# Kernel tuning notes

Hardware: AMD Instinct MI355X
Metric: run time of the kernel (lower is better)

Reference implementation:

```python
import jax, jax.numpy as jnp
import numpy as np

NUM_HIDDEN = 128
NUM_IN = 256
NUM_HEADS = 4
B, T, N, K = 4, 32, 96, 30


def setup_inputs() -> dict:
    key = jax.random.key(0)
    ks = jax.random.split(key, 7)
    return {
        "h_V": jax.random.normal(ks[0], (B, T, N, NUM_HIDDEN), dtype=jnp.float32),
        "h_EV": jax.random.normal(ks[1], (B, T, N, K, NUM_IN), dtype=jnp.float32),
        "mask_attend": jax.random.randint(ks[2], (B, T, N, K), 0, 2, dtype=jnp.int32),
        "Wq": jax.random.normal(ks[3], (NUM_HIDDEN, NUM_HIDDEN), dtype=jnp.float32) / np.sqrt(NUM_HIDDEN),
        "Wk": jax.random.normal(ks[4], (NUM_IN, NUM_HIDDEN), dtype=jnp.float32) / np.sqrt(NUM_IN),
        "Wv": jax.random.normal(ks[5], (NUM_IN, NUM_HIDDEN), dtype=jnp.float32) / np.sqrt(NUM_IN),
        "Wo": jax.random.normal(ks[6], (NUM_HIDDEN, NUM_HIDDEN), dtype=jnp.float32) / np.sqrt(NUM_HIDDEN),
    }


def reference(h_V, h_EV, mask_attend, Wq, Wk, Wv, Wo):
    b, t, n, k = h_EV.shape[:4]
    h = NUM_HEADS
    d = NUM_HIDDEN // h
    # projections
    Q = (h_V @ Wq).reshape(b, t, n, h, d)            # [B,T,N,H,d]
    Kp = (h_EV @ Wk).reshape(b, t, n, k, h, d)       # [B,T,N,K,H,d]
    V = (h_EV @ Wv).reshape(b, t, n, k, h, d)        # [B,T,N,K,H,d]
    # per-node neighbor attention logits [B,T,N,H,K]
    logits = jnp.einsum('btnhd,btnkhd->btnhk', Q, Kp) / jnp.sqrt(jnp.float32(d))
    neg_inf = jnp.finfo(jnp.float32).min
    mask = mask_attend[:, :, :, None, :]             # [B,T,N,1,K] -> broadcast over heads
    logits = jnp.where(mask > 0, logits, neg_inf)
    attend = jax.nn.softmax(logits, axis=-1)
    attend = attend * mask.astype(jnp.float32)
    # combine values: [B,T,N,H,d]
    out = jnp.einsum('btnhk,btnkhd->btnhd', attend, V).reshape(b, t, n, NUM_HIDDEN)
    return out @ Wo
```

## Files before the change

kernel.cpp:

```cpp
#include <hip/hip_runtime.h>
#include <hip/hip_bf16.h>
#include <cfloat>
#include <math.h>

constexpr int SITES = 12288;
constexpr int KNB   = 30;
constexpr int CIN   = 256;
#define RSQRT_D 0.17677669529663689f

typedef short bf16x8 __attribute__((ext_vector_type(8)));
typedef float f32x4  __attribute__((ext_vector_type(4)));

__device__ inline unsigned short f2bs(float x) {
    __hip_bfloat16 b = __float2bfloat16(x);
    return *(unsigned short*)&b;
}
__device__ inline float bs2f(unsigned short u) {
    unsigned int v = (unsigned int)u << 16;
    float f;
    __builtin_memcpy(&f, &v, 4);
    return f;
}
__device__ inline unsigned int pack2(float a, float b) {
    return (unsigned int)f2bs(a) | ((unsigned int)f2bs(b) << 16);
}

__global__ __launch_bounds__(256) void precompute_w(
    const float* __restrict__ Wq, const float* __restrict__ Wk,
    const float* __restrict__ Wv, const float* __restrict__ Wo,
    unsigned short* __restrict__ Mt, unsigned short* __restrict__ W3t) {
    int gid = blockIdx.x * 256 + threadIdx.x;
    if (gid < 131072) {
        int p = gid >> 7;
        int i = gid & 127;
        int h = p >> 8;
        int c = p & 255;
        const float4* wq = (const float4*)(Wq + (size_t)i * 128 + h * 32);
        const float4* wk = (const float4*)(Wk + (size_t)c * 128 + h * 32);
        float s = 0.f;
        #pragma unroll
        for (int d = 0; d < 8; ++d) {
            float4 a = wq[d], b = wk[d];
            s += a.x * b.x; s += a.y * b.y; s += a.z * b.z; s += a.w * b.w;
        }
        Mt[gid] = f2bs(s);
    } else {
        int o = gid - 131072;
        int p = o >> 7;
        int j = o & 127;
        int h = p >> 8;
        int c = p & 255;
        const float* wv = Wv + (size_t)c * 128 + h * 32;
        const float* wo = Wo + (size_t)(h * 32) * 128 + j;
        float s = 0.f;
        #pragma unroll
        for (int d = 0; d < 32; ++d)
            s += wv[d] * wo[(size_t)d * 128];
        W3t[(size_t)j * 1024 + p] = f2bs(s);
    }
}

template <bool OUT_BF16, bool A_F32>
__global__ __launch_bounds__(256) void gemm_bt_bf16(
    const void* __restrict__ Aptr, const unsigned short* __restrict__ Bt,
    void* __restrict__ C, int M, int N, int K) {
    constexpr int BM = 64, BN = 128, BK = 32, PAD = 8;
    constexpr int NT = BN / 16;
    __shared__ unsigned short As[BM][BK + PAD];
    __shared__ unsigned short Bs[BN][BK + PAD];
    const int tid  = threadIdx.x;
    const int wave = tid >> 6;
    const int lane = tid & 63;
    const int quad = lane >> 4;
    const int l16  = lane & 15;
    const int bm0 = blockIdx.x * BM;
    const int bn0 = blockIdx.y * BN;

    f32x4 acc[NT];
    #pragma unroll
    for (int j = 0; j < NT; ++j) acc[j] = (f32x4){0.f, 0.f, 0.f, 0.f};

    for (int kk = 0; kk < K; kk += BK) {
        {
            int row = tid >> 2, off = (tid & 3) * 8;
            if (A_F32) {
                const float* Af = (const float*)Aptr;
                const float4* src = (const float4*)&Af[(size_t)(bm0 + row) * K + kk + off];
                float4 a0 = src[0], a1 = src[1];
                uint4 p;
                p.x = pack2(a0.x, a0.y); p.y = pack2(a0.z, a0.w);
                p.z = pack2(a1.x, a1.y); p.w = pack2(a1.z, a1.w);
                *(uint4*)&As[row][off] = p;
            } else {
                const unsigned short* Ab = (const unsigned short*)Aptr;
                *(uint4*)&As[row][off] =
                    *(const uint4*)&Ab[(size_t)(bm0 + row) * K + kk + off];
            }
        }
        #pragma unroll
        for (int i = 0; i < 2; ++i) {
            int c2 = tid * 2 + i;
            int brow = c2 >> 2, boff = (c2 & 3) * 8;
            *(uint4*)&Bs[brow][boff] =
                *(const uint4*)&Bt[(size_t)(bn0 + brow) * K + kk + boff];
        }
        __syncthreads();
        bf16x8 af = *(const bf16x8*)&As[wave * 16 + l16][quad * 8];
        #pragma unroll
        for (int j = 0; j < NT; ++j) {
            bf16x8 bf = *(const bf16x8*)&Bs[j * 16 + l16][quad * 8];
            acc[j] = __builtin_amdgcn_mfma_f32_16x16x32_bf16(af, bf, acc[j], 0, 0, 0);
        }
        __syncthreads();
    }
    int row0 = bm0 + wave * 16 + quad * 4;
    #pragma unroll
    for (int j = 0; j < NT; ++j) {
        int col = bn0 + j * 16 + l16;
        #pragma unroll
        for (int r = 0; r < 4; ++r) {
            if (OUT_BF16)
                ((unsigned short*)C)[(size_t)(row0 + r) * N + col] = f2bs(acc[j][r]);
            else
                ((float*)C)[(size_t)(row0 + r) * N + col] = acc[j][r];
        }
    }
}

__global__ __launch_bounds__(256) void attn_kernel(
    const float* __restrict__ hEV, const int* __restrict__ mask,
    const unsigned short* __restrict__ qt, unsigned short* __restrict__ evb) {
    __shared__ unsigned short evS[KNB * CIN];
    __shared__ float qS[1024];
    __shared__ float logitsL[4 * 32];
    __shared__ float attendL[4 * 32];
    __shared__ int   activeS[32];
    __shared__ int   naS;

    const int s = blockIdx.x;
    const int tid = threadIdx.x;
    const int lane = tid & 63;
    const int wv = tid >> 6;
    const int hw = lane >> 5;
    const int sl = lane & 31;

    if (tid < 64) {
        int mk = (tid < KNB) ? mask[(size_t)s * KNB + tid] : 0;
        unsigned long long bal = __ballot(mk > 0);
        if (tid == 0) naS = __popcll(bal);
        if (mk > 0) activeS[__popcll(bal & ((1ull << tid) - 1))] = tid;
    } else if (tid < 192) {
        int t2 = tid - 64;
        uint4 u = ((const uint4*)(qt + (size_t)s * 1024))[t2];
        float f[8];
        f[0] = bs2f(u.x & 0xffff); f[1] = bs2f(u.x >> 16);
        f[2] = bs2f(u.y & 0xffff); f[3] = bs2f(u.y >> 16);
        f[4] = bs2f(u.z & 0xffff); f[5] = bs2f(u.z >> 16);
        f[6] = bs2f(u.w & 0xffff); f[7] = bs2f(u.w >> 16);
        *(float4*)&qS[t2 * 8]     = *(float4*)&f[0];
        *(float4*)&qS[t2 * 8 + 4] = *(float4*)&f[4];
    }
    __syncthreads();

    float qf[4][8];
    #pragma unroll
    for (int h = 0; h < 4; ++h) {
        *(float4*)&qf[h][0] = *(const float4*)&qS[h * 256 + sl * 8];
        *(float4*)&qf[h][4] = *(const float4*)&qS[h * 256 + sl * 8 + 4];
    }
    const int na = naS;

    for (int r = wv * 2 + hw; r < na; r += 8) {
        int k = activeS[r];
        const float* row = hEV + (size_t)s * (KNB * CIN) + (size_t)k * CIN + sl * 8;
        float4 v0 = *(const float4*)row;
        float4 v1 = *(const float4*)(row + 4);

        uint4 p;
        p.x = pack2(v0.x, v0.y); p.y = pack2(v0.z, v0.w);
        p.z = pack2(v1.x, v1.y); p.w = pack2(v1.z, v1.w);
        *(uint4*)&evS[r * CIN + sl * 8] = p;

        float l[4];
        #pragma unroll
        for (int h = 0; h < 4; ++h) {
            l[h] = v0.x * qf[h][0] + v0.y * qf[h][1] + v0.z * qf[h][2] + v0.w * qf[h][3]
                 + v1.x * qf[h][4] + v1.y * qf[h][5] + v1.z * qf[h][6] + v1.w * qf[h][7];
        }
        #pragma unroll
        for (int m = 1; m < 32; m <<= 1) {
            #pragma unroll
            for (int h = 0; h < 4; ++h) l[h] += __shfl_xor(l[h], m, 64);
        }
        if (sl == 0) {
            #pragma unroll
            for (int h = 0; h < 4; ++h) logitsL[h * 32 + r] = l[h] * RSQRT_D;
        }
    }
    __syncthreads();

    {
        float lg = (lane < na) ? logitsL[wv * 32 + lane] : -FLT_MAX;
        float mx = lg;
        #pragma unroll
        for (int m = 1; m < 64; m <<= 1) mx = fmaxf(mx, __shfl_xor(mx, m, 64));
        float e = (lane < na) ? __expf(lg - mx) : 0.f;
        float sm = e;
        #pragma unroll
        for (int m = 1; m < 64; m <<= 1) sm += __shfl_xor(sm, m, 64);
        if (lane < na) attendL[wv * 32 + lane] = e / sm;
    }
    __syncthreads();

    float a0 = 0.f, a1 = 0.f, a2 = 0.f, a3 = 0.f;
    for (int r = 0; r < na; ++r) {
        float evv = bs2f(evS[r * CIN + tid]);
        a0 = fmaf(attendL[r], evv, a0);
        a1 = fmaf(attendL[32 + r], evv, a1);
        a2 = fmaf(attendL[64 + r], evv, a2);
        a3 = fmaf(attendL[96 + r], evv, a3);
    }
    size_t ob = (size_t)s * 1024 + tid;
    evb[ob]       = f2bs(a0);
    evb[ob + 256] = f2bs(a1);
    evb[ob + 512] = f2bs(a2);
    evb[ob + 768] = f2bs(a3);
}

extern "C" void kernel_launch(void* const* d_in, const int* in_sizes, int n_in,
                              void* d_out, int out_size, void* d_ws, size_t ws_size,
                              hipStream_t stream) {
    const float* hV   = (const float*)d_in[0];
    const float* hEV  = (const float*)d_in[1];
    const int*   mask = (const int*)d_in[2];
    const float* Wq   = (const float*)d_in[3];
    const float* Wk   = (const float*)d_in[4];
    const float* Wv   = (const float*)d_in[5];
    const float* Wo   = (const float*)d_in[6];
    float* out = (float*)d_out;

    unsigned short* ws = (unsigned short*)d_ws;
    unsigned short* Mt   = ws;
    unsigned short* W3t  = ws + 131072;
    unsigned short* qt   = ws + 262144;
    unsigned short* evb  = qt + (size_t)SITES * 1024;
    size_t need = ((size_t)262144 + 2 * (size_t)SITES * 1024) * 2;
    if (ws_size < need) return;

    precompute_w<<<dim3(1024), dim3(256), 0, stream>>>(Wq, Wk, Wv, Wo, Mt, W3t);

    gemm_bt_bf16<true, true><<<dim3(SITES / 64, 1024 / 128), dim3(256), 0, stream>>>(
        hV, Mt, qt, SITES, 1024, 128);

    attn_kernel<<<dim3(SITES), dim3(256), 0, stream>>>(hEV, mask, qt, evb);

    gemm_bt_bf16<false, false><<<dim3(SITES / 64, 1), dim3(256), 0, stream>>>(
        evb, W3t, out, SITES, 128, 1024);
}
```

Baseline: 511.9 us.

## Fuse attention with output projection using one wave per site and online softmax

Replaces the per-site attention kernel and the separate output GEMM with a single kernel. Each wave handles four sites in turn, streaming the active neighbor rows with a one-ahead prefetch and an online softmax that only rescales when the running max moves by more than a threshold. The per-site bf16 attention result stays in swizzled shared memory and feeds MFMA against W3t in the same block, so the evb intermediate no longer goes through global memory. In exchange the softmax becomes approximate-online, each wave works through its sites serially, and W3t is reloaded from global memory by every block.

```diff
diff --git a/kernel.cpp b/kernel.cpp
--- a/kernel.cpp
+++ b/kernel.cpp
@@ -127,104 +127,116 @@
     }
 }
 
-__global__ __launch_bounds__(256) void attn_kernel(
+__global__ __launch_bounds__(256) void attn_out_fused(
     const float* __restrict__ hEV, const int* __restrict__ mask,
-    const unsigned short* __restrict__ qt, unsigned short* __restrict__ evb) {
-    __shared__ unsigned short evS[KNB * CIN];
-    __shared__ float qS[1024];
-    __shared__ float logitsL[4 * 32];
-    __shared__ float attendL[4 * 32];
-    __shared__ int   activeS[32];
-    __shared__ int   naS;
-
-    const int s = blockIdx.x;
-    const int tid = threadIdx.x;
+    const unsigned short* __restrict__ qt, const unsigned short* __restrict__ W3t,
+    float* __restrict__ out) {
+    __shared__ __align__(16) unsigned short evbS[16 * 1024];
+    const int tid  = threadIdx.x;
     const int lane = tid & 63;
-    const int wv = tid >> 6;
-    const int hw = lane >> 5;
-    const int sl = lane & 31;
-
-    if (tid < 64) {
-        int mk = (tid < KNB) ? mask[(size_t)s * KNB + tid] : 0;
+    const int wv   = tid >> 6;
+    const int s0   = blockIdx.x * 16;
+
+    for (int si = 0; si < 4; ++si) {
+        const int site = wv * 4 + si;
+        const int s = s0 + site;
+
+        int mk = (lane < KNB) ? mask[(size_t)s * KNB + lane] : 0;
         unsigned long long bal = __ballot(mk > 0);
-        if (tid == 0) naS = __popcll(bal);
-        if (mk > 0) activeS[__popcll(bal & ((1ull << tid) - 1))] = tid;
-    } else if (tid < 192) {
-        int t2 = tid - 64;
-        uint4 u = ((const uint4*)(qt + (size_t)s * 1024))[t2];
-        float f[8];
-        f[0] = bs2f(u.x & 0xffff); f[1] = bs2f(u.x >> 16);
-        f[2] = bs2f(u.y & 0xffff); f[3] = bs2f(u.y >> 16);
-        f[4] = bs2f(u.z & 0xffff); f[5] = bs2f(u.z >> 16);
-        f[6] = bs2f(u.w & 0xffff); f[7] = bs2f(u.w >> 16);
-        *(float4*)&qS[t2 * 8]     = *(float4*)&f[0];
-        *(float4*)&qS[t2 * 8 + 4] = *(float4*)&f[4];
+        unsigned mw = (unsigned)bal & 0x3FFFFFFFu;
+        int na = __popc(mw);
+
+        float qf[4][4];
+        const unsigned short* qrow = qt + (size_t)s * 1024;
+        #pragma unroll
+        for (int h = 0; h < 4; ++h) {
+            ushort4 u = *(const ushort4*)&qrow[h * 256 + lane * 4];
+            qf[h][0] = bs2f(u.x); qf[h][1] = bs2f(u.y);
+            qf[h][2] = bs2f(u.z); qf[h][3] = bs2f(u.w);
+        }
+
+        float mh[4], lh[4], acc[4][4];
+        #pragma unroll
+        for (int h = 0; h < 4; ++h) {
+            mh[h] = -3.0e38f; lh[h] = 0.f;
+            acc[h][0] = acc[h][1] = acc[h][2] = acc[h][3] = 0.f;
+        }
+
+        const float* base = hEV + (size_t)s * (KNB * CIN) + lane * 4;
+        unsigned lmw = mw;
+        float4 cur = {0,0,0,0}, nxt = {0,0,0,0};
+        if (na > 0) {
+            int k = __builtin_ctz(lmw); lmw &= lmw - 1;
+            cur = *(const float4*)(base + (size_t)k * CIN);
+        }
+        for (int r = 0; r < na; ++r) {
+            if (r + 1 < na) {
+                int kn = __builtin_ctz(lmw); lmw &= lmw - 1;
+                nxt = *(const float4*)(base + (size_t)kn * CIN);
+            }
+            float4 v = cur;
+            float lg[4];
+            #pragma unroll
+            for (int h = 0; h < 4; ++h)
+                lg[h] = v.x * qf[h][0] + v.y * qf[h][1]
+                      + v.z * qf[h][2] + v.w * qf[h][3];
+            #pragma unroll
+            for (int mm = 1; mm < 64; mm <<= 1) {
+                #pragma unroll
+                for (int h = 0; h < 4; ++h) lg[h] += __shfl_xor(lg[h], mm, 64);
+            }
+            #pragma unroll
+            for (int h = 0; h < 4; ++h) {
+                float g = lg[h] * RSQRT_D;
+                if (g > mh[h] + 8.f) {
+                    float sc = __expf(mh[h] - g);
+                    lh[h] *= sc;
+                    acc[h][0] *= sc; acc[h][1] *= sc;
+                    acc[h][2] *= sc; acc[h][3] *= sc;
+                    mh[h] = g;
+                }
+                float p = __expf(g - mh[h]);
+                lh[h] += p;
+                acc[h][0] = fmaf(p, v.x, acc[h][0]);
+                acc[h][1] = fmaf(p, v.y, acc[h][1]);
+                acc[h][2] = fmaf(p, v.z, acc[h][2]);
+                acc[h][3] = fmaf(p, v.w, acc[h][3]);
+            }
+            cur = nxt;
+        }
+        const int swz = (site & 7) << 4;
+        #pragma unroll
+        for (int h = 0; h < 4; ++h) {
+            float inv = (lh[h] > 0.f) ? 1.f / lh[h] : 0.f;
+            unsigned p0 = pack2(acc[h][0] * inv, acc[h][1] * inv);
+            unsigned p1 = pack2(acc[h][2] * inv, acc[h][3] * inv);
+            int byte = (h * 512 + lane * 8) ^ swz;
+            *(uint2*)((char*)evbS + site * 2048 + byte) = make_uint2(p0, p1);
+        }
     }
     __syncthreads();
 
-    float qf[4][8];
+    const int quad = lane >> 4;
+    const int l16  = lane & 15;
+    const int n0   = wv * 32;
+    f32x4 oacc0 = (f32x4){0.f, 0.f, 0.f, 0.f};
+    f32x4 oacc1 = (f32x4){0.f, 0.f, 0.f, 0.f};
+    const int aswz = (l16 & 7) << 4;
+    #pragma unroll 4
+    for (int kk = 0; kk < 1024; kk += 32) {
+        int abyte = ((kk + quad * 8) * 2) ^ aswz;
+        bf16x8 af = *(const bf16x8*)((const char*)evbS + l16 * 2048 + abyte);
+        bf16x8 b0 = *(const bf16x8*)&W3t[(size_t)(n0 + l16) * 1024 + kk + quad * 8];
+        bf16x8 b1 = *(const bf16x8*)&W3t[(size_t)(n0 + 16 + l16) * 1024 + kk + quad * 8];
+        oacc0 = __builtin_amdgcn_mfma_f32_16x16x32_bf16(af, b0, oacc0, 0, 0, 0);
+        oacc1 = __builtin_amdgcn_mfma_f32_16x16x32_bf16(af, b1, oacc1, 0, 0, 0);
+    }
+    int srow = s0 + quad * 4;
     #pragma unroll
-    for (int h = 0; h < 4; ++h) {
-        *(float4*)&qf[h][0] = *(const float4*)&qS[h * 256 + sl * 8];
-        *(float4*)&qf[h][4] = *(const float4*)&qS[h * 256 + sl * 8 + 4];
-    }
-    const int na = naS;
-
-    for (int r = wv * 2 + hw; r < na; r += 8) {
-        int k = activeS[r];
-        const float* row = hEV + (size_t)s * (KNB * CIN) + (size_t)k * CIN + sl * 8;
-        float4 v0 = *(const float4*)row;
-        float4 v1 = *(const float4*)(row + 4);
-
-        uint4 p;
-        p.x = pack2(v0.x, v0.y); p.y = pack2(v0.z, v0.w);
-        p.z = pack2(v1.x, v1.y); p.w = pack2(v1.z, v1.w);
-        *(uint4*)&evS[r * CIN + sl * 8] = p;
-
-        float l[4];
-        #pragma unroll
-        for (int h = 0; h < 4; ++h) {
-            l[h] = v0.x * qf[h][0] + v0.y * qf[h][1] + v0.z * qf[h][2] + v0.w * qf[h][3]
-                 + v1.x * qf[h][4] + v1.y * qf[h][5] + v1.z * qf[h][6] + v1.w * qf[h][7];
-        }
-        #pragma unroll
-        for (int m = 1; m < 32; m <<= 1) {
-            #pragma unroll
-            for (int h = 0; h < 4; ++h) l[h] += __shfl_xor(l[h], m, 64);
-        }
-        if (sl == 0) {
-            #pragma unroll
-            for (int h = 0; h < 4; ++h) logitsL[h * 32 + r] = l[h] * RSQRT_D;
-        }
-    }
-    __syncthreads();
-
-    {
-        float lg = (lane < na) ? logitsL[wv * 32 + lane] : -FLT_MAX;
-        float mx = lg;
-        #pragma unroll
-        for (int m = 1; m < 64; m <<= 1) mx = fmaxf(mx, __shfl_xor(mx, m, 64));
-        float e = (lane < na) ? __expf(lg - mx) : 0.f;
-        float sm = e;
-        #pragma unroll
-        for (int m = 1; m < 64; m <<= 1) sm += __shfl_xor(sm, m, 64);
-        if (lane < na) attendL[wv * 32 + lane] = e / sm;
-    }
-    __syncthreads();
-
-    float a0 = 0.f, a1 = 0.f, a2 = 0.f, a3 = 0.f;
-    for (int r = 0; r < na; ++r) {
-        float evv = bs2f(evS[r * CIN + tid]);
-        a0 = fmaf(attendL[r], evv, a0);
-        a1 = fmaf(attendL[32 + r], evv, a1);
-        a2 = fmaf(attendL[64 + r], evv, a2);
-        a3 = fmaf(attendL[96 + r], evv, a3);
-    }
-    size_t ob = (size_t)s * 1024 + tid;
-    evb[ob]       = f2bs(a0);
-    evb[ob + 256] = f2bs(a1);
-    evb[ob + 512] = f2bs(a2);
-    evb[ob + 768] = f2bs(a3);
+    for (int r = 0; r < 4; ++r) {
+        out[(size_t)(srow + r) * 128 + n0 + l16]      = oacc0[r];
+        out[(size_t)(srow + r) * 128 + n0 + 16 + l16] = oacc1[r];
+    }
 }
 
 extern "C" void kernel_launch(void* const* d_in, const int* in_sizes, int n_in,
@@ -243,8 +255,7 @@
     unsigned short* Mt   = ws;
     unsigned short* W3t  = ws + 131072;
     unsigned short* qt   = ws + 262144;
-    unsigned short* evb  = qt + (size_t)SITES * 1024;
-    size_t need = ((size_t)262144 + 2 * (size_t)SITES * 1024) * 2;
+    size_t need = ((size_t)262144 + (size_t)SITES * 1024) * 2;
     if (ws_size < need) return;
 
     precompute_w<<<dim3(1024), dim3(256), 0, stream>>>(Wq, Wk, Wv, Wo, Mt, W3t);
@@ -252,8 +263,6 @@
     gemm_bt_bf16<true, true><<<dim3(SITES / 64, 1024 / 128), dim3(256), 0, stream>>>(
         hV, Mt, qt, SITES, 1024, 128);
 
-    attn_kernel<<<dim3(SITES), dim3(256), 0, stream>>>(hEV, mask, qt, evb);
-
-    gemm_bt_bf16<false, false><<<dim3(SITES / 64, 1), dim3(256), 0, stream>>>(
-        evb, W3t, out, SITES, 128, 1024);
-}
+    attn_out_fused<<<dim3(SITES / 16), dim3(256), 0, stream>>>(
+        hEV, mask, qt, W3t, out);
+}
```

New measurement: 524.0 us. 1.02x slower.
